# Optimization experiments

Measured on AMD Instinct MI355X. Metric: run time of the kernel, lower is better.

## Reference

```python
import jax, jax.numpy as jnp
import numpy as np

N, E, G = 32768, 262144, 1024
FIN, ED = 32, 8
H, C = 4, 64            # gat_heads, graph_hidden_dim
HC = H * C              # 256
FP_IN, DESC_IN = 2048, 200
GOUT, FPOUT, DOUT = 64, 256, 64
TIN = GOUT + FPOUT + DOUT  # 384
NT = 12
BN_EPS = 1e-5


def bn_eval(x, gamma, beta):
    # eval-mode BatchNorm1d with default running stats (mean=0, var=1)
    inv = 1.0 / jnp.sqrt(1.0 + BN_EPS)
    return x * (gamma * inv) + beta


def gatv2(x, edge_index, edge_attr, Wl, bl, Wr, br, We, att, bias):
    """PyG GATv2Conv (concat heads, add_self_loops=True, fill_value='mean')."""
    n = x.shape[0]
    src, dst = edge_index[0], edge_index[1]
    # self-loop edge_attr = mean of incoming edge_attr per node (PyG fill_value='mean')
    deg = jax.ops.segment_sum(jnp.ones(src.shape, x.dtype), dst, n)
    ea_loop = jax.ops.segment_sum(edge_attr, dst, n) / jnp.maximum(deg, 1.0)[:, None]
    loop = jnp.arange(n)
    src = jnp.concatenate([src, loop])
    dst = jnp.concatenate([dst, loop])
    ea = jnp.concatenate([edge_attr, ea_loop], axis=0)
    xl = (x @ Wl + bl).reshape(n, H, C)   # source transform
    xr = (x @ Wr + br).reshape(n, H, C)   # target transform
    ee = (ea @ We).reshape(-1, H, C)      # edge transform (no bias in PyG)
    m = jax.nn.leaky_relu(xl[src] + xr[dst] + ee, 0.2)  # [E', H, C]
    logit = jnp.einsum('ehc,hc->eh', m, att)            # [E', H]
    # segment softmax over incoming edges of each target node
    lmax = jax.ops.segment_max(logit, dst, n)
    p = jnp.exp(logit - lmax[dst])
    alpha = p / jax.ops.segment_sum(p, dst, n)[dst]
    out = jax.ops.segment_sum(xl[src] * alpha[:, :, None], dst, n)  # [n, H, C]
    return out.reshape(n, HC) + bias


def setup_inputs() -> dict:
    key = jax.random.key(0)
    ks = iter(jax.random.split(key, 64))

    def p(shape, scale=0.05):
        return jax.random.normal(next(ks), shape, dtype=jnp.float32) * scale

    inp = {}
    inp['x'] = jax.random.normal(next(ks), (N, FIN), dtype=jnp.float32)
    inp['edge_index'] = jax.random.randint(next(ks), (2, E), 0, N, dtype=jnp.int32)
    inp['edge_attr'] = jax.random.normal(next(ks), (E, ED), dtype=jnp.float32)
    inp['batch'] = (jnp.arange(N) * G) // N          # sorted, covers all G graphs
    inp['fp'] = jax.random.uniform(next(ks), (G, FP_IN), dtype=jnp.float32)
    inp['desc'] = jax.random.normal(next(ks), (G, DESC_IN), dtype=jnp.float32)
    # GATv2 layer 1 (in=FIN) and layer 2 (in=HC)
    for tag, fin in (('c1', FIN), ('c2', HC)):
        inp[tag + '_Wl'] = p((fin, HC))
        inp[tag + '_bl'] = p((HC,))
        inp[tag + '_Wr'] = p((fin, HC))
        inp[tag + '_br'] = p((HC,))
        inp[tag + '_We'] = p((ED, HC))
        inp[tag + '_att'] = p((H, C))
        inp[tag + '_bias'] = p((HC,))
    inp['gW'], inp['gb'] = p((HC, GOUT)), p((GOUT,))
    inp['g_gn'], inp['g_bt'] = jnp.ones((GOUT,)), jnp.zeros((GOUT,))
    inp['fW'], inp['fb'] = p((FP_IN, FPOUT)), p((FPOUT,))
    inp['f_gn'], inp['f_bt'] = jnp.ones((FPOUT,)), jnp.zeros((FPOUT,))
    inp['dW'], inp['db'] = p((DESC_IN, DOUT)), p((DOUT,))
    inp['d_gn'], inp['d_bt'] = jnp.ones((DOUT,)), jnp.zeros((DOUT,))
    inp['k1W'], inp['k1b'] = p((TIN, TIN // 2)), p((TIN // 2,))
    inp['k1_gn'], inp['k1_bt'] = jnp.ones((TIN // 2,)), jnp.zeros((TIN // 2,))
    inp['k2W'], inp['k2b'] = p((TIN // 2, TIN // 4)), p((TIN // 4,))
    inp['k2_gn'], inp['k2_bt'] = jnp.ones((TIN // 4,)), jnp.zeros((TIN // 4,))
    inp['k3W'], inp['k3b'] = p((TIN // 4, NT)), p((NT,))
    return inp


def reference(x, edge_index, edge_attr, batch, fp, desc,
              c1_Wl, c1_bl, c1_Wr, c1_br, c1_We, c1_att, c1_bias,
              c2_Wl, c2_bl, c2_Wr, c2_br, c2_We, c2_att, c2_bias,
              gW, gb, g_gn, g_bt, fW, fb, f_gn, f_bt, dW, db, d_gn, d_bt,
              k1W, k1b, k1_gn, k1_bt, k2W, k2b, k2_gn, k2_bt, k3W, k3b):
    h = jax.nn.relu(gatv2(x, edge_index, edge_attr, c1_Wl, c1_bl, c1_Wr, c1_br, c1_We, c1_att, c1_bias))
    h = jax.nn.relu(gatv2(h, edge_index, edge_attr, c2_Wl, c2_bl, c2_Wr, c2_br, c2_We, c2_att, c2_bias))
    xg = jax.ops.segment_max(h, batch, G)                 # global_max_pool
    xg = bn_eval(jax.nn.relu(xg @ gW + gb), g_gn, g_bt)
    xf = bn_eval(jax.nn.relu(fp @ fW + fb), f_gn, f_bt)
    xd = bn_eval(jax.nn.relu(desc @ dW + db), d_gn, d_bt)
    z = jnp.concatenate([xg, xf, xd], axis=1)             # [G, TIN]
    z = bn_eval(jax.nn.relu(z @ k1W + k1b), k1_gn, k1_bt)  # dropout off (eval)
    z = bn_eval(jax.nn.relu(z @ k2W + k2b), k2_gn, k2_bt)
    return z @ k3W + k3b                                  # [G, NT]
```

## Files before the change

### kernel.cpp

```cpp
#include <hip/hip_runtime.h>
#include <hip/hip_bf16.h>
#include <math.h>

#define NHEAD 4
#define HC 256

typedef short short8 __attribute__((ext_vector_type(8)));
typedef short short4v __attribute__((ext_vector_type(4)));
typedef float f32x4 __attribute__((ext_vector_type(4)));

__device__ inline f32x4 bf4_to_f32(short4v v)
{
  f32x4 r;
#pragma unroll
  for (int i = 0; i < 4; ++i)
    r[i] = __uint_as_float(((unsigned)(unsigned short)v[i]) << 16);
  return r;
}

__device__ inline float bf_to_f32(unsigned short u)
{
  return __uint_as_float(((unsigned)u) << 16);
}

__device__ inline short4v f4_to_bf4(f32x4 v)
{
  short4v o;
#pragma unroll
  for (int i = 0; i < 4; ++i) {
    __hip_bfloat16 h = __float2bfloat16(v[i]);
    o[i] = *(short*)&h;
  }
  return o;
}

template <int CTRL>
__device__ inline float dpp_radd(float x)
{
  int yi = __builtin_amdgcn_update_dpp(0, __float_as_int(x), CTRL, 0xf, 0xf, true);
  return x + __int_as_float(yi);
}

__global__ void prep_kernel(
    const float* __restrict__ x, const float* __restrict__ fp,
    const float* __restrict__ c1Wl, const float* __restrict__ c1Wr,
    const float* __restrict__ c2Wl, const float* __restrict__ c2Wr,
    const float* __restrict__ desc, const float* __restrict__ dW,
    const float* __restrict__ k1W, const float* __restrict__ fW,
    const int* __restrict__ dst, int* __restrict__ deg,
    __hip_bfloat16* __restrict__ xbf, __hip_bfloat16* __restrict__ fpbf,
    __hip_bfloat16* __restrict__ wt1, __hip_bfloat16* __restrict__ wt2,
    __hip_bfloat16* __restrict__ descbf, __hip_bfloat16* __restrict__ dwt,
    __hip_bfloat16* __restrict__ k1wt, __hip_bfloat16* __restrict__ fwt,
    int N, int G, int E, int DIN)
{
  const int n0 = N * 8;
  const int n1 = G * 512;
  const int n2 = 512 * 32, n3 = 512 * 256;
  const int n4 = G * 224, n5 = 64 * 224, n6 = 192 * 384;
  const int n7 = 256 * 2048;
  int idx = blockIdx.x * 256 + threadIdx.x;
  if (idx < n0) {
    f32x4 v = ((const f32x4*)x)[idx];
    ((short4v*)xbf)[idx] = f4_to_bf4(v);
    return;
  }
  idx -= n0;
  if (idx < n1) {
    f32x4 v = ((const f32x4*)fp)[idx];
    ((short4v*)fpbf)[idx] = f4_to_bf4(v);
    return;
  }
  idx -= n1;
  if (idx < n2) {
    int n = idx / 32, k = idx - n * 32;
    float v = (n < 256) ? c1Wl[k * 256 + n] : c1Wr[k * 256 + (n - 256)];
    wt1[idx] = __float2bfloat16(v); return;
  }
  idx -= n2;
  if (idx < n3) {
    int n = idx / 256, k = idx - n * 256;
    float v = (n < 256) ? c2Wl[k * 256 + n] : c2Wr[k * 256 + (n - 256)];
    wt2[idx] = __float2bfloat16(v); return;
  }
  idx -= n3;
  if (idx < n4) {
    int row = idx / 224, kp = idx - row * 224;
    float v = (kp < DIN) ? desc[(long)row * DIN + kp] : 0.f;
    descbf[idx] = __float2bfloat16(v); return;
  }
  idx -= n4;
  if (idx < n5) {
    int n = idx / 224, kp = idx - n * 224;
    float v = (kp < DIN) ? dW[kp * 64 + n] : 0.f;
    dwt[idx] = __float2bfloat16(v); return;
  }
  idx -= n5;
  if (idx < n6) {
    int n = idx / 384, k = idx - n * 384;
    k1wt[idx] = __float2bfloat16(k1W[k * 192 + n]); return;
  }
  idx -= n6;
  if (idx < n7) {
    int n = idx >> 11, k = idx & 2047;
    fwt[idx] = __float2bfloat16(fW[k * 256 + n]); return;
  }
  idx -= n7;
  if (idx < E) atomicAdd(&deg[dst[idx]], 1);
}

__global__ __launch_bounds__(256) void gemm_mfma_kernel(
    const __hip_bfloat16* __restrict__ A, const __hip_bfloat16* __restrict__ BT,
    const float* __restrict__ bl, const float* __restrict__ br,
    __hip_bfloat16* __restrict__ XL, __hip_bfloat16* __restrict__ XR, int M, int K)
{
  __shared__ short As[128 * 40];
  __shared__ short Bs[128 * 40];
  int bm = blockIdx.x * 128, bn = blockIdx.y * 128;
  int t = threadIdx.x;
  int w = t >> 6, l = t & 63;
  int quad = l >> 4, l16 = l & 15;
  int srow = t >> 1, scol = (t & 1) * 16;

  f32x4 acc[2][8];
#pragma unroll
  for (int i = 0; i < 2; ++i)
#pragma unroll
    for (int j = 0; j < 8; ++j) acc[i][j] = (f32x4){0.f, 0.f, 0.f, 0.f};

  for (int k0 = 0; k0 < K; k0 += 32) {
    *(short8*)&As[srow * 40 + scol] =
        *(const short8*)(const void*)&A[(long)(bm + srow) * K + k0 + scol];
    *(short8*)&As[srow * 40 + scol + 8] =
        *(const short8*)(const void*)&A[(long)(bm + srow) * K + k0 + scol + 8];
    *(short8*)&Bs[srow * 40 + scol] =
        *(const short8*)(const void*)&BT[(long)(bn + srow) * K + k0 + scol];
    *(short8*)&Bs[srow * 40 + scol + 8] =
        *(const short8*)(const void*)&BT[(long)(bn + srow) * K + k0 + scol + 8];
    __syncthreads();
    short8 af[2], bf[8];
#pragma unroll
    for (int mt = 0; mt < 2; ++mt)
      af[mt] = *(short8*)&As[(w * 32 + mt * 16 + l16) * 40 + quad * 8];
#pragma unroll
    for (int nt = 0; nt < 8; ++nt)
      bf[nt] = *(short8*)&Bs[(nt * 16 + l16) * 40 + quad * 8];
#pragma unroll
    for (int mt = 0; mt < 2; ++mt)
#pragma unroll
      for (int nt = 0; nt < 8; ++nt)
        acc[mt][nt] = __builtin_amdgcn_mfma_f32_16x16x32_bf16(af[mt], bf[nt], acc[mt][nt], 0, 0, 0);
    __syncthreads();
  }
#pragma unroll
  for (int mt = 0; mt < 2; ++mt)
#pragma unroll
    for (int nt = 0; nt < 8; ++nt) {
      int col = bn + nt * 16 + l16;
      float b = (col < 256) ? bl[col] : br[col - 256];
#pragma unroll
      for (int r = 0; r < 4; ++r) {
        int row = bm + w * 32 + mt * 16 + quad * 4 + r;
        float v = acc[mt][nt][r] + b;
        if (col < 256)
          XL[(long)row * 256 + col] = __float2bfloat16(v);
        else
          XR[(long)row * 256 + (col - 256)] = __float2bfloat16(v);
      }
    }
}

__global__ __launch_bounds__(256) void gemm_rb_kernel(
    const __hip_bfloat16* __restrict__ A, const __hip_bfloat16* __restrict__ BT,
    const float* __restrict__ bias, const float* __restrict__ gamma,
    const float* __restrict__ beta, void* __restrict__ out,
    int M, int K, int ldc, int coloff, int obf)
{
  __shared__ short As[64 * 40];
  __shared__ short Bs[64 * 40];
  int bm = blockIdx.x * 64, bn = blockIdx.y * 64;
  int t = threadIdx.x;
  int w = t >> 6, l = t & 63;
  int quad = l >> 4, l16 = l & 15;
  int lrow = t >> 2, col8 = (t & 3) * 8;

  f32x4 acc[4];
#pragma unroll
  for (int nt = 0; nt < 4; ++nt) acc[nt] = (f32x4){0.f, 0.f, 0.f, 0.f};

  for (int k0 = 0; k0 < K; k0 += 32) {
    *(short8*)&As[lrow * 40 + col8] =
        *(const short8*)(const void*)&A[(long)(bm + lrow) * K + k0 + col8];
    *(short8*)&Bs[lrow * 40 + col8] =
        *(const short8*)(const void*)&BT[(long)(bn + lrow) * K + k0 + col8];
    __syncthreads();
    short8 af = *(short8*)&As[(w * 16 + l16) * 40 + quad * 8];
#pragma unroll
    for (int nt = 0; nt < 4; ++nt) {
      short8 bf = *(short8*)&Bs[(nt * 16 + l16) * 40 + quad * 8];
      acc[nt] = __builtin_amdgcn_mfma_f32_16x16x32_bf16(af, bf, acc[nt], 0, 0, 0);
    }
    __syncthreads();
  }
  const float inv = rsqrtf(1.f + 1e-5f);
#pragma unroll
  for (int nt = 0; nt < 4; ++nt) {
    int col = bn + nt * 16 + l16;
    float b = bias[col], gm = gamma[col] * inv, bt = beta[col];
#pragma unroll
    for (int r = 0; r < 4; ++r) {
      int row = bm + w * 16 + quad * 4 + r;
      float v = fmaxf(acc[nt][r] + b, 0.f) * gm + bt;
      if (obf)
        ((__hip_bfloat16*)out)[(long)row * ldc + coloff + col] = __float2bfloat16(v);
      else
        ((float*)out)[(long)row * ldc + coloff + col] = v;
    }
  }
}

__global__ __launch_bounds__(256) void mega1_kernel(
    const __hip_bfloat16* __restrict__ fpbf, const __hip_bfloat16* __restrict__ fwt,
    float* __restrict__ P,
    const int* __restrict__ esrc, const int* __restrict__ edst,
    const float* __restrict__ ea, int* __restrict__ cursor,
    int* __restrict__ csr_src, float* __restrict__ csr_ea,
    const __hip_bfloat16* __restrict__ descbf, const __hip_bfloat16* __restrict__ dwt,
    const float* __restrict__ db, const float* __restrict__ d_gn,
    const float* __restrict__ d_bt, __hip_bfloat16* __restrict__ zbuf,
    int G, int E)
{
  __shared__ short As[64 * 40];
  __shared__ short Bs[64 * 40];
  int b = blockIdx.x;
  const int t = threadIdx.x;
  const int NB_SKB = (G / 64) * 16;
  const int NB_FILL = E / 256;

  if (b < NB_SKB) {
    const int gx = G / 64;
    int bx = b % gx, rem = b / gx;
    int by = rem & 3, s = rem >> 2;
    int bm = bx * 64, bn = by * 64;
    const int K = 2048, Kc = 512;
    int kb = s * Kc, ke = kb + Kc;
    int w = t >> 6, l = t & 63;
    int quad = l >> 4, l16 = l & 15;
    int lrow = t >> 2, col8 = (t & 3) * 8;

    f32x4 acc[4];
#pragma unroll
    for (int nt = 0; nt < 4; ++nt) acc[nt] = (f32x4){0.f, 0.f, 0.f, 0.f};

    for (int k0 = kb; k0 < ke; k0 += 32) {
      *(short8*)&As[lrow * 40 + col8] =
          *(const short8*)(const void*)&fpbf[(long)(bm + lrow) * K + k0 + col8];
      *(short8*)&Bs[lrow * 40 + col8] =
          *(const short8*)(const void*)&fwt[(long)(bn + lrow) * K + k0 + col8];
      __syncthreads();
      short8 af = *(short8*)&As[(w * 16 + l16) * 40 + quad * 8];
#pragma unroll
      for (int nt = 0; nt < 4; ++nt) {
        short8 bf = *(short8*)&Bs[(nt * 16 + l16) * 40 + quad * 8];
        acc[nt] = __builtin_amdgcn_mfma_f32_16x16x32_bf16(af, bf, acc[nt], 0, 0, 0);
      }
      __syncthreads();
    }
#pragma unroll
    for (int nt = 0; nt < 4; ++nt) {
      int col = bn + nt * 16 + l16;
#pragma unroll
      for (int r = 0; r < 4; ++r) {
        int row = bm + w * 16 + quad * 4 + r;
        P[((long)s * G + row) * 256 + col] = acc[nt][r];
      }
    }
    return;
  }
  b -= NB_SKB;
  if (b < NB_FILL) {
    int e = b * 256 + t;
    if (e < E) {
      int pos = atomicAdd(&cursor[edst[e]], 1);
      csr_src[pos] = esrc[e];
      f32x4 a0 = *(const f32x4*)(const void*)&ea[(long)e * 8];
      f32x4 a1 = *(const f32x4*)(const void*)&ea[(long)e * 8 + 4];
      *(f32x4*)&csr_ea[(long)pos * 8] = a0;
      *(f32x4*)&csr_ea[(long)pos * 8 + 4] = a1;
    }
    return;
  }
  b -= NB_FILL;
  {
    int bm = b * 64;
    const int K = 224;
    int w = t >> 6, l = t & 63;
    int quad = l >> 4, l16 = l & 15;
    int lrow = t >> 2, col8 = (t & 3) * 8;

    f32x4 acc[4];
#pragma unroll
    for (int nt = 0; nt < 4; ++nt) acc[nt] = (f32x4){0.f, 0.f, 0.f, 0.f};

    for (int k0 = 0; k0 < K; k0 += 32) {
      *(short8*)&As[lrow * 40 + col8] =
          *(const short8*)(const void*)&descbf[(long)(bm + lrow) * K + k0 + col8];
      *(short8*)&Bs[lrow * 40 + col8] =
          *(const short8*)(const void*)&dwt[(long)lrow * K + k0 + col8];
      __syncthreads();
      short8 af = *(short8*)&As[(w * 16 + l16) * 40 + quad * 8];
#pragma unroll
      for (int nt = 0; nt < 4; ++nt) {
        short8 bf = *(short8*)&Bs[(nt * 16 + l16) * 40 + quad * 8];
        acc[nt] = __builtin_amdgcn_mfma_f32_16x16x32_bf16(af, bf, acc[nt], 0, 0, 0);
      }
      __syncthreads();
    }
    const float inv = rsqrtf(1.f + 1e-5f);
#pragma unroll
    for (int nt = 0; nt < 4; ++nt) {
      int col = nt * 16 + l16;
      float bb = db[col], gm = d_gn[col] * inv, bt = d_bt[col];
#pragma unroll
      for (int r = 0; r < 4; ++r) {
        int row = bm + w * 16 + quad * 4 + r;
        float v = fmaxf(acc[nt][r] + bb, 0.f) * gm + bt;
        zbuf[(long)row * 384 + 320 + col] = __float2bfloat16(v);
      }
    }
  }
}

__global__ __launch_bounds__(256) void mega2_kernel(
    const float* __restrict__ csr_ea, const int* __restrict__ csr_ptr,
    float* __restrict__ ea_mean,
    const float* __restrict__ P, const float* __restrict__ fb,
    const float* __restrict__ f_gn, const float* __restrict__ f_bt,
    __hip_bfloat16* __restrict__ zbuf, int N, int G)
{
  int b = blockIdx.x;
  int t = threadIdx.x;
  const int NB_EA = N * 8 / 256;
  if (b < NB_EA) {
    int idx = b * 256 + t;
    int node = idx >> 3, d = idx & 7;
    int p0 = csr_ptr[node], p1 = csr_ptr[node + 1];
    float s = 0.f;
    for (int k = p0; k < p1; ++k) s += csr_ea[(long)k * 8 + d];
    int cnt = p1 - p0;
    ea_mean[idx] = s / (float)(cnt > 1 ? cnt : 1);
    return;
  }
  b -= NB_EA;
  int idx = b * 256 + t;
  int row = idx >> 8, col = idx & 255;
  float v = 0.f;
#pragma unroll
  for (int s = 0; s < 4; ++s) v += P[(long)s * G * 256 + idx];
  const float inv = rsqrtf(1.f + 1e-5f);
  v = fmaxf(v + fb[col], 0.f) * (f_gn[col] * inv) + f_bt[col];
  zbuf[(long)row * 384 + 64 + col] = __float2bfloat16(v);
}

__global__ __launch_bounds__(256) void poolg_kernel(
    const __hip_bfloat16* __restrict__ h, const float* __restrict__ gW,
    const float* __restrict__ gb, const float* __restrict__ g_gn,
    const float* __restrict__ g_bt, __hip_bfloat16* __restrict__ zbuf, int npg)
{
  __shared__ float smax[256];
  __shared__ float sred[256];
  int g = blockIdx.x, t = threadIdx.x;
  const __hip_bfloat16* base = h + (long)g * npg * HC + t;
  float m = -INFINITY;
#pragma unroll 4
  for (int i = 0; i < npg; ++i)
    m = fmaxf(m, bf_to_f32(*(const unsigned short*)&base[(long)i * HC]));
  smax[t] = m;
  __syncthreads();
  int j = t >> 2, part = t & 3;
  float sum = 0.f;
#pragma unroll 4
  for (int k = part * 64; k < part * 64 + 64; ++k)
    sum = fmaf(smax[k], gW[k * 64 + j], sum);
  sred[t] = sum;
  __syncthreads();
  if (t < 64) {
    float v = sred[t * 4] + sred[t * 4 + 1] + sred[t * 4 + 2] + sred[t * 4 + 3];
    const float inv = rsqrtf(1.f + 1e-5f);
    v = fmaxf(v + gb[t], 0.f) * (g_gn[t] * inv) + g_bt[t];
    zbuf[(long)g * 384 + t] = __float2bfloat16(v);
  }
}

__global__ __launch_bounds__(256) void head23_kernel(
    const float* __restrict__ z1, const float* __restrict__ k2W,
    const float* __restrict__ k2b, const float* __restrict__ k2_gn,
    const float* __restrict__ k2_bt, const float* __restrict__ k3W,
    const float* __restrict__ k3b, float* __restrict__ out)
{
  __shared__ float sW[96 * 96];
  __shared__ float s1[8 * 192];
  __shared__ float s2[8 * 96];
  __shared__ float sk3[96 * 12];
  int b = blockIdx.x, t = threadIdx.x;

  for (int i = t; i < 8 * 192; i += 256) s1[i] = z1[(long)b * (8 * 192) + i];
  for (int i = t; i < 96 * 12; i += 256) sk3[i] = k3W[i];

  int row[3], col[3];
  float acc[3] = {0.f, 0.f, 0.f};
#pragma unroll
  for (int o = 0; o < 3; ++o) {
    int idx = o * 256 + t;
    row[o] = idx / 96;
    col[o] = idx - row[o] * 96;
  }

  for (int half = 0; half < 2; ++half) {
    __syncthreads();
    for (int i = t; i < 96 * 96; i += 256)
      sW[i] = k2W[(long)half * 96 * 96 + i];
    __syncthreads();
#pragma unroll 4
    for (int k = 0; k < 96; ++k) {
#pragma unroll
      for (int o = 0; o < 3; ++o)
        acc[o] = fmaf(s1[row[o] * 192 + half * 96 + k], sW[k * 96 + col[o]], acc[o]);
    }
  }

  const float inv = rsqrtf(1.f + 1e-5f);
#pragma unroll
  for (int o = 0; o < 3; ++o) {
    float v = fmaxf(acc[o] + k2b[col[o]], 0.f) * (k2_gn[col[o]] * inv) + k2_bt[col[o]];
    s2[o * 256 + t] = v;
  }
  __syncthreads();
  if (t < 96) {
    int r3 = t / 12, c3 = t - r3 * 12;
    float a = 0.f;
#pragma unroll 4
    for (int k = 0; k < 96; ++k) a = fmaf(s2[r3 * 96 + k], sk3[k * 12 + c3], a);
    out[(long)(b * 8 + r3) * 12 + c3] = a + k3b[c3];
  }
}

__global__ __launch_bounds__(1024) void scan1_kernel(
    const int* __restrict__ deg, int* __restrict__ ptr,
    int* __restrict__ bsum, int N)
{
  __shared__ int s[1024];
  int b = blockIdx.x, t = threadIdx.x;
  int i = b * 1024 + t;
  int v = (i < N) ? deg[i] : 0;
  s[t] = v;
  __syncthreads();
  for (int off = 1; off < 1024; off <<= 1) {
    int x = (t >= off) ? s[t - off] : 0;
    __syncthreads();
    s[t] += x;
    __syncthreads();
  }
  if (i < N) ptr[i] = s[t] - v;
  if (t == 1023) bsum[b] = s[1023];
}

__global__ __launch_bounds__(256) void scan2_kernel(
    const int* __restrict__ bsum, int* __restrict__ ptr,
    int* __restrict__ cursor, int N, int nb)
{
  int i = blockIdx.x * 256 + threadIdx.x;
  if (i > N) return;
  if (i == N) {
    int tot = 0;
    for (int j = 0; j < nb; ++j) tot += bsum[j];
    ptr[N] = tot;
    return;
  }
  int b = i >> 10;
  int offv = 0;
  for (int j = 0; j < b; ++j) offv += bsum[j];
  int v = ptr[i] + offv;
  ptr[i] = v;
  cursor[i] = v;
}

__global__ __launch_bounds__(128) void gat_kernel(
    const __hip_bfloat16* __restrict__ xlb, const __hip_bfloat16* __restrict__ xrb,
    const float* __restrict__ csr_ea, const int* __restrict__ csr_src,
    const int* __restrict__ csr_ptr, const float* __restrict__ ea_mean,
    const float* __restrict__ We, const float* __restrict__ att,
    const float* __restrict__ bias, __hip_bfloat16* __restrict__ out, int N)
{
  int lane = threadIdx.x & 63;
  int node = blockIdx.x * 2 + (threadIdx.x >> 6);
  if (node >= N) return;
  int cbase = (lane >> 4) * 64 + (lane & 15) * 4;

  f32x4 attv = *(const f32x4*)(const void*)&att[cbase];
  f32x4 xriv = bf4_to_f32(*(const short4v*)(const void*)&xrb[(long)node * HC + cbase]);
  f32x4 WeR[8];
#pragma unroll
  for (int d = 0; d < 8; ++d)
    WeR[d] = *(const f32x4*)(const void*)&We[d * HC + cbase];

  float rsumA = 0.f, rsumB = 0.f;
  f32x4 accA = (f32x4){0.f, 0.f, 0.f, 0.f};
  f32x4 accB = (f32x4){0.f, 0.f, 0.f, 0.f};

  int p0 = csr_ptr[node], p1 = csr_ptr[node + 1];

  auto edge_compute = [&](f32x4 xls, f32x4 ea0, f32x4 ea1,
                          float& rsum, f32x4& acc) {
    f32x4 mv = xriv + xls;
#pragma unroll
    for (int d = 0; d < 4; ++d) mv += WeR[d] * ea0[d];
#pragma unroll
    for (int d = 0; d < 4; ++d) mv += WeR[d + 4] * ea1[d];
    float t = 0.f;
#pragma unroll
    for (int r = 0; r < 4; ++r) {
      float m = mv[r];
      m = (m > 0.f) ? m : 0.2f * m;
      t = fmaf(m, attv[r], t);
    }
    t = dpp_radd<0x121>(t);
    t = dpp_radd<0x122>(t);
    t = dpp_radd<0x124>(t);
    t = dpp_radd<0x128>(t);
    float p = __expf(t);
    rsum += p;
    acc += p * xls;
  };

  short4v xA = (short4v){0, 0, 0, 0}, xB = xA, xC = xA;
  f32x4 a0A = (f32x4){0.f, 0.f, 0.f, 0.f}, a1A = a0A;
  f32x4 a0B = a0A, a1B = a0A, a0C = a0A, a1C = a0A;
  int s3A = 0, s3B = 0, s3C = 0;

  int s0 = 0, s1 = 0, s2 = 0;
  if (p0 < p1)     s0 = csr_src[p0];
  if (p0 + 1 < p1) s1 = csr_src[p0 + 1];
  if (p0 + 2 < p1) s2 = csr_src[p0 + 2];
  if (p0 + 3 < p1) s3A = csr_src[p0 + 3];
  if (p0 + 4 < p1) s3B = csr_src[p0 + 4];
  if (p0 + 5 < p1) s3C = csr_src[p0 + 5];
  if (p0 < p1) {
    a0A = *(const f32x4*)(const void*)&csr_ea[(long)p0 * 8];
    a1A = *(const f32x4*)(const void*)&csr_ea[(long)p0 * 8 + 4];
    xA = *(const short4v*)(const void*)&xlb[(long)s0 * HC + cbase];
  }
  if (p0 + 1 < p1) {
    a0B = *(const f32x4*)(const void*)&csr_ea[(long)(p0 + 1) * 8];
    a1B = *(const f32x4*)(const void*)&csr_ea[(long)(p0 + 1) * 8 + 4];
    xB = *(const short4v*)(const void*)&xlb[(long)s1 * HC + cbase];
  }
  if (p0 + 2 < p1) {
    a0C = *(const f32x4*)(const void*)&csr_ea[(long)(p0 + 2) * 8];
    a1C = *(const f32x4*)(const void*)&csr_ea[(long)(p0 + 2) * 8 + 4];
    xC = *(const short4v*)(const void*)&xlb[(long)s2 * HC + cbase];
  }

  int k = p0;
  for (; k + 3 <= p1; k += 3) {
    f32x4 e0 = a0A, e1 = a1A;
    short4v xc = xA;
    if (k + 3 < p1) {
      xA = *(const short4v*)(const void*)&xlb[(long)s3A * HC + cbase];
      a0A = *(const f32x4*)(const void*)&csr_ea[(long)(k + 3) * 8];
      a1A = *(const f32x4*)(const void*)&csr_ea[(long)(k + 3) * 8 + 4];
    }
    if (k + 6 < p1) s3A = csr_src[k + 6];
    edge_compute(bf4_to_f32(xc), e0, e1, rsumA, accA);

    e0 = a0B; e1 = a1B; xc = xB;
    if (k + 4 < p1) {
      xB = *(const short4v*)(const void*)&xlb[(long)s3B * HC + cbase];
      a0B = *(const f32x4*)(const void*)&csr_ea[(long)(k + 4) * 8];
      a1B = *(const f32x4*)(const void*)&csr_ea[(long)(k + 4) * 8 + 4];
    }
    if (k + 7 < p1) s3B = csr_src[k + 7];
    edge_compute(bf4_to_f32(xc), e0, e1, rsumB, accB);

    e0 = a0C; e1 = a1C; xc = xC;
    if (k + 5 < p1) {
      xC = *(const short4v*)(const void*)&xlb[(long)s3C * HC + cbase];
      a0C = *(const f32x4*)(const void*)&csr_ea[(long)(k + 5) * 8];
      a1C = *(const f32x4*)(const void*)&csr_ea[(long)(k + 5) * 8 + 4];
    }
    if (k + 8 < p1) s3C = csr_src[k + 8];
    edge_compute(bf4_to_f32(xc), e0, e1, rsumA, accA);
  }
  if (k < p1)     edge_compute(bf4_to_f32(xA), a0A, a1A, rsumA, accA);
  if (k + 1 < p1) edge_compute(bf4_to_f32(xB), a0B, a1B, rsumB, accB);

  f32x4 em0 = *(const f32x4*)(const void*)&ea_mean[(long)node * 8];
  f32x4 em1 = *(const f32x4*)(const void*)&ea_mean[(long)node * 8 + 4];
  f32x4 xls_self = bf4_to_f32(*(const short4v*)(const void*)&xlb[(long)node * HC + cbase]);
  edge_compute(xls_self, em0, em1, rsumB, accB);

  float invs = 1.f / (rsumA + rsumB);
  f32x4 biasv = *(const f32x4*)(const void*)&bias[cbase];
  short4v pk;
#pragma unroll
  for (int r = 0; r < 4; ++r) {
    float v = fmaxf((accA[r] + accB[r]) * invs + biasv[r], 0.f);
    __hip_bfloat16 hv = __float2bfloat16(v);
    pk[r] = *(short*)&hv;
  }
  *(short4v*)&out[(long)node * HC + cbase] = pk;
}

extern "C" void kernel_launch(void* const* d_in, const int* in_sizes, int n_in,
                              void* d_out, int out_size, void* d_ws, size_t ws_size,
                              hipStream_t stream)
{
  const float* x          = (const float*)d_in[0];
  const int*   edge_index = (const int*)d_in[1];
  const float* edge_attr  = (const float*)d_in[2];
  const float* fp         = (const float*)d_in[4];
  const float* desc       = (const float*)d_in[5];
  const float *c1_Wl = (const float*)d_in[6],  *c1_bl = (const float*)d_in[7],
              *c1_Wr = (const float*)d_in[8],  *c1_br = (const float*)d_in[9],
              *c1_We = (const float*)d_in[10], *c1_att = (const float*)d_in[11],
              *c1_bias = (const float*)d_in[12];
  const float *c2_Wl = (const float*)d_in[13], *c2_bl = (const float*)d_in[14],
              *c2_Wr = (const float*)d_in[15], *c2_br = (const float*)d_in[16],
              *c2_We = (const float*)d_in[17], *c2_att = (const float*)d_in[18],
              *c2_bias = (const float*)d_in[19];
  const float *gW = (const float*)d_in[20], *gb = (const float*)d_in[21],
              *g_gn = (const float*)d_in[22], *g_bt = (const float*)d_in[23];
  const float *fW = (const float*)d_in[24], *fb = (const float*)d_in[25],
              *f_gn = (const float*)d_in[26], *f_bt = (const float*)d_in[27];
  const float *dW = (const float*)d_in[28], *db = (const float*)d_in[29],
              *d_gn = (const float*)d_in[30], *d_bt = (const float*)d_in[31];
  const float *k1W = (const float*)d_in[32], *k1b = (const float*)d_in[33],
              *k1_gn = (const float*)d_in[34], *k1_bt = (const float*)d_in[35];
  const float *k2W = (const float*)d_in[36], *k2b = (const float*)d_in[37],
              *k2_gn = (const float*)d_in[38], *k2_bt = (const float*)d_in[39];
  const float *k3W = (const float*)d_in[40], *k3b = (const float*)d_in[41];

  const int N = in_sizes[0] / 32;
  const int E = in_sizes[1] / 2;
  const int G = in_sizes[4] / 2048;
  const int FIN = 32, FPIN = 2048;
  const int DIN = in_sizes[5] / G;

  char* ws = (char*)d_ws;
  size_t off = 0;
  auto alloc = [&](size_t bytes) {
    void* p = ws + off;
    off = (off + bytes + 255) & ~(size_t)255;
    return p;
  };
  __hip_bfloat16* xlb    = (__hip_bfloat16*)alloc((size_t)N * HC * 2);
  __hip_bfloat16* xrb    = (__hip_bfloat16*)alloc((size_t)N * HC * 2);
  __hip_bfloat16* hb1    = (__hip_bfloat16*)alloc((size_t)N * HC * 2);
  __hip_bfloat16* hb2    = (__hip_bfloat16*)alloc((size_t)N * HC * 2);
  __hip_bfloat16* xbf    = (__hip_bfloat16*)alloc((size_t)N * FIN * 2);
  __hip_bfloat16* fpbf   = (__hip_bfloat16*)alloc((size_t)G * FPIN * 2);
  __hip_bfloat16* wt1    = (__hip_bfloat16*)alloc((size_t)512 * FIN * 2);
  __hip_bfloat16* wt2    = (__hip_bfloat16*)alloc((size_t)512 * HC * 2);
  __hip_bfloat16* fwt    = (__hip_bfloat16*)alloc((size_t)256 * FPIN * 2);
  __hip_bfloat16* descbf = (__hip_bfloat16*)alloc((size_t)G * 224 * 2);
  __hip_bfloat16* dwt    = (__hip_bfloat16*)alloc((size_t)64 * 224 * 2);
  __hip_bfloat16* k1wt   = (__hip_bfloat16*)alloc((size_t)192 * 384 * 2);
  __hip_bfloat16* zbuf   = (__hip_bfloat16*)alloc((size_t)G * 384 * 2);
  float* z1      = (float*)alloc((size_t)G * 192 * 4);
  float* P_fp    = (float*)alloc((size_t)4 * G * 256 * 4);
  int*   deg     = (int*)alloc((size_t)N * 4);
  int*   csr_ptr = (int*)alloc((size_t)(N + 1) * 4);
  int*   cursor  = (int*)alloc((size_t)N * 4);
  int*   csr_src = (int*)alloc((size_t)E * 4);
  float* csr_ea  = (float*)alloc((size_t)E * 8 * 4);
  float* ea_mean = (float*)alloc((size_t)N * 8 * 4);
  int*   bsum    = (int*)alloc((size_t)64 * 4);
  (void)ws_size;

  const int* srcp = edge_index;
  const int* dstp = edge_index + E;
  const int nb = (N + 1023) / 1024;

  hipMemsetAsync(deg, 0, (size_t)N * 4, stream);

  {
    long total = (long)N * 8 + (long)G * 512 + 512 * 32 + 512 * 256 +
                 (long)G * 224 + 64 * 224 + 192 * 384 + 256 * 2048 + E;
    prep_kernel<<<(int)((total + 255) / 256), 256, 0, stream>>>(
        x, fp, c1_Wl, c1_Wr, c2_Wl, c2_Wr, desc, dW, k1W, fW, dstp, deg,
        xbf, fpbf, wt1, wt2, descbf, dwt, k1wt, fwt, N, G, E, DIN);
  }
  scan1_kernel<<<nb, 1024, 0, stream>>>(deg, csr_ptr, bsum, N);
  scan2_kernel<<<(N + 1 + 255) / 256, 256, 0, stream>>>(bsum, csr_ptr, cursor, N, nb);

  {
    int nblk = (G / 64) * 16 + E / 256 + G / 64;
    mega1_kernel<<<nblk, 256, 0, stream>>>(
        fpbf, fwt, P_fp, srcp, dstp, edge_attr, cursor, csr_src, csr_ea,
        descbf, dwt, db, d_gn, d_bt, zbuf, G, E);
  }

  gemm_mfma_kernel<<<dim3(N / 128, 4), 256, 0, stream>>>(xbf, wt1, c1_bl, c1_br, xlb, xrb, N, FIN);

  mega2_kernel<<<N * 8 / 256 + G, 256, 0, stream>>>(
      csr_ea, csr_ptr, ea_mean, P_fp, fb, f_gn, f_bt, zbuf, N, G);

  gat_kernel<<<N / 2, 128, 0, stream>>>(xlb, xrb, csr_ea, csr_src, csr_ptr, ea_mean,
                                        c1_We, c1_att, c1_bias, hb1, N);
  gemm_mfma_kernel<<<dim3(N / 128, 4), 256, 0, stream>>>(hb1, wt2, c2_bl, c2_br, xlb, xrb, N, HC);
  gat_kernel<<<N / 2, 128, 0, stream>>>(xlb, xrb, csr_ea, csr_src, csr_ptr, ea_mean,
                                        c2_We, c2_att, c2_bias, hb2, N);

  poolg_kernel<<<G, 256, 0, stream>>>(hb2, gW, gb, g_gn, g_bt, zbuf, N / G);

  gemm_rb_kernel<<<dim3(G / 64, 3), 256, 0, stream>>>(zbuf, k1wt, k1b, k1_gn, k1_bt,
                                                      z1, G, 384, 192, 0, 0);
  head23_kernel<<<G / 8, 256, 0, stream>>>(z1, k2W, k2b, k2_gn, k2_bt, k3W, k3b,
                                           (float*)d_out);
}
```

Baseline: 388.6 us.

## Fuse layer-1 GEMM into mega1 and collapse pooling plus MLP head into one kernel

Result: slower. 403.0 us (+3.7%).

```diff
diff --git a/kernel.cpp b/kernel.cpp
--- a/kernel.cpp
+++ b/kernel.cpp
@@ -46,19 +46,19 @@
     const float* __restrict__ c1Wl, const float* __restrict__ c1Wr,
     const float* __restrict__ c2Wl, const float* __restrict__ c2Wr,
     const float* __restrict__ desc, const float* __restrict__ dW,
-    const float* __restrict__ k1W, const float* __restrict__ fW,
+    const float* __restrict__ fW,
     const int* __restrict__ dst, int* __restrict__ deg,
     __hip_bfloat16* __restrict__ xbf, __hip_bfloat16* __restrict__ fpbf,
     __hip_bfloat16* __restrict__ wt1, __hip_bfloat16* __restrict__ wt2,
     __hip_bfloat16* __restrict__ descbf, __hip_bfloat16* __restrict__ dwt,
-    __hip_bfloat16* __restrict__ k1wt, __hip_bfloat16* __restrict__ fwt,
+    __hip_bfloat16* __restrict__ fwt,
     int N, int G, int E, int DIN)
 {
   const int n0 = N * 8;
   const int n1 = G * 512;
   const int n2 = 512 * 32, n3 = 512 * 256;
-  const int n4 = G * 224, n5 = 64 * 224, n6 = 192 * 384;
-  const int n7 = 256 * 2048;
+  const int n4 = G * 224, n5 = 64 * 224;
+  const int n6 = 256 * 2048;
   int idx = blockIdx.x * 256 + threadIdx.x;
   if (idx < n0) {
     f32x4 v = ((const f32x4*)x)[idx];
@@ -97,15 +97,10 @@
   }
   idx -= n5;
   if (idx < n6) {
-    int n = idx / 384, k = idx - n * 384;
-    k1wt[idx] = __float2bfloat16(k1W[k * 192 + n]); return;
-  }
-  idx -= n6;
-  if (idx < n7) {
     int n = idx >> 11, k = idx & 2047;
     fwt[idx] = __float2bfloat16(fW[k * 256 + n]); return;
   }
-  idx -= n7;
+  idx -= n6;
   if (idx < E) atomicAdd(&deg[dst[idx]], 1);
 }
 
@@ -170,73 +165,99 @@
     }
 }
 
-__global__ __launch_bounds__(256) void gemm_rb_kernel(
-    const __hip_bfloat16* __restrict__ A, const __hip_bfloat16* __restrict__ BT,
-    const float* __restrict__ bias, const float* __restrict__ gamma,
-    const float* __restrict__ beta, void* __restrict__ out,
-    int M, int K, int ldc, int coloff, int obf)
-{
-  __shared__ short As[64 * 40];
-  __shared__ short Bs[64 * 40];
-  int bm = blockIdx.x * 64, bn = blockIdx.y * 64;
-  int t = threadIdx.x;
-  int w = t >> 6, l = t & 63;
-  int quad = l >> 4, l16 = l & 15;
-  int lrow = t >> 2, col8 = (t & 3) * 8;
-
-  f32x4 acc[4];
-#pragma unroll
-  for (int nt = 0; nt < 4; ++nt) acc[nt] = (f32x4){0.f, 0.f, 0.f, 0.f};
-
-  for (int k0 = 0; k0 < K; k0 += 32) {
-    *(short8*)&As[lrow * 40 + col8] =
-        *(const short8*)(const void*)&A[(long)(bm + lrow) * K + k0 + col8];
-    *(short8*)&Bs[lrow * 40 + col8] =
-        *(const short8*)(const void*)&BT[(long)(bn + lrow) * K + k0 + col8];
-    __syncthreads();
-    short8 af = *(short8*)&As[(w * 16 + l16) * 40 + quad * 8];
-#pragma unroll
-    for (int nt = 0; nt < 4; ++nt) {
-      short8 bf = *(short8*)&Bs[(nt * 16 + l16) * 40 + quad * 8];
-      acc[nt] = __builtin_amdgcn_mfma_f32_16x16x32_bf16(af, bf, acc[nt], 0, 0, 0);
-    }
-    __syncthreads();
-  }
-  const float inv = rsqrtf(1.f + 1e-5f);
-#pragma unroll
-  for (int nt = 0; nt < 4; ++nt) {
-    int col = bn + nt * 16 + l16;
-    float b = bias[col], gm = gamma[col] * inv, bt = beta[col];
-#pragma unroll
-    for (int r = 0; r < 4; ++r) {
-      int row = bm + w * 16 + quad * 4 + r;
-      float v = fmaxf(acc[nt][r] + b, 0.f) * gm + bt;
-      if (obf)
-        ((__hip_bfloat16*)out)[(long)row * ldc + coloff + col] = __float2bfloat16(v);
-      else
-        ((float*)out)[(long)row * ldc + coloff + col] = v;
-    }
-  }
-}
-
 __global__ __launch_bounds__(256) void mega1_kernel(
-    const __hip_bfloat16* __restrict__ fpbf, const __hip_bfloat16* __restrict__ fwt,
-    float* __restrict__ P,
     const int* __restrict__ esrc, const int* __restrict__ edst,
     const float* __restrict__ ea, int* __restrict__ cursor,
     int* __restrict__ csr_src, float* __restrict__ csr_ea,
+    const __hip_bfloat16* __restrict__ xbf, const __hip_bfloat16* __restrict__ wt1,
+    const float* __restrict__ c1_bl, const float* __restrict__ c1_br,
+    __hip_bfloat16* __restrict__ xlb, __hip_bfloat16* __restrict__ xrb,
+    const __hip_bfloat16* __restrict__ fpbf, const __hip_bfloat16* __restrict__ fwt,
+    float* __restrict__ P,
     const __hip_bfloat16* __restrict__ descbf, const __hip_bfloat16* __restrict__ dwt,
     const float* __restrict__ db, const float* __restrict__ d_gn,
     const float* __restrict__ d_bt, __hip_bfloat16* __restrict__ zbuf,
-    int G, int E)
-{
-  __shared__ short As[64 * 40];
-  __shared__ short Bs[64 * 40];
+    int N, int G, int E)
+{
+  __shared__ short As[128 * 40];
+  __shared__ short Bs[128 * 40];
   int b = blockIdx.x;
   const int t = threadIdx.x;
+  const int NB_FILL = E / 256;
+  const int GX1 = N / 128;
+  const int NB_GEMM1 = GX1 * 4;
   const int NB_SKB = (G / 64) * 16;
-  const int NB_FILL = E / 256;
-
+
+  if (b < NB_FILL) {
+    int e = b * 256 + t;
+    if (e < E) {
+      int pos = atomicAdd(&cursor[edst[e]], 1);
+      csr_src[pos] = esrc[e];
+      f32x4 a0 = *(const f32x4*)(const void*)&ea[(long)e * 8];
+      f32x4 a1 = *(const f32x4*)(const void*)&ea[(long)e * 8 + 4];
+      *(f32x4*)&csr_ea[(long)pos * 8] = a0;
+      *(f32x4*)&csr_ea[(long)pos * 8 + 4] = a1;
+    }
+    return;
+  }
+  b -= NB_FILL;
+  if (b < NB_GEMM1) {
+    int bx = b % GX1, by = b / GX1;
+    int bm = bx * 128, bn = by * 128;
+    const int K = 32;
+    int w = t >> 6, l = t & 63;
+    int quad = l >> 4, l16 = l & 15;
+    int srow = t >> 1, scol = (t & 1) * 16;
+
+    f32x4 acc[2][8];
+#pragma unroll
+    for (int i = 0; i < 2; ++i)
+#pragma unroll
+      for (int j = 0; j < 8; ++j) acc[i][j] = (f32x4){0.f, 0.f, 0.f, 0.f};
+
+    {
+      const int k0 = 0;
+      *(short8*)&As[srow * 40 + scol] =
+          *(const short8*)(const void*)&xbf[(long)(bm + srow) * K + k0 + scol];
+      *(short8*)&As[srow * 40 + scol + 8] =
+          *(const short8*)(const void*)&xbf[(long)(bm + srow) * K + k0 + scol + 8];
+      *(short8*)&Bs[srow * 40 + scol] =
+          *(const short8*)(const void*)&wt1[(long)(bn + srow) * K + k0 + scol];
+      *(short8*)&Bs[srow * 40 + scol + 8] =
+          *(const short8*)(const void*)&wt1[(long)(bn + srow) * K + k0 + scol + 8];
+      __syncthreads();
+      short8 af[2], bf[8];
+#pragma unroll
+      for (int mt = 0; mt < 2; ++mt)
+        af[mt] = *(short8*)&As[(w * 32 + mt * 16 + l16) * 40 + quad * 8];
+#pragma unroll
+      for (int nt = 0; nt < 8; ++nt)
+        bf[nt] = *(short8*)&Bs[(nt * 16 + l16) * 40 + quad * 8];
+#pragma unroll
+      for (int mt = 0; mt < 2; ++mt)
+#pragma unroll
+        for (int nt = 0; nt < 8; ++nt)
+          acc[mt][nt] = __builtin_amdgcn_mfma_f32_16x16x32_bf16(af[mt], bf[nt], acc[mt][nt], 0, 0, 0);
+    }
+#pragma unroll
+    for (int mt = 0; mt < 2; ++mt)
+#pragma unroll
+      for (int nt = 0; nt < 8; ++nt) {
+        int col = bn + nt * 16 + l16;
+        float bb = (col < 256) ? c1_bl[col] : c1_br[col - 256];
+#pragma unroll
+        for (int r = 0; r < 4; ++r) {
+          int row = bm + w * 32 + mt * 16 + quad * 4 + r;
+          float v = acc[mt][nt][r] + bb;
+          if (col < 256)
+            xlb[(long)row * 256 + col] = __float2bfloat16(v);
+          else
+            xrb[(long)row * 256 + (col - 256)] = __float2bfloat16(v);
+        }
+      }
+    return;
+  }
+  b -= NB_GEMM1;
   if (b < NB_SKB) {
     const int gx = G / 64;
     int bx = b % gx, rem = b / gx;
@@ -278,19 +299,6 @@
     return;
   }
   b -= NB_SKB;
-  if (b < NB_FILL) {
-    int e = b * 256 + t;
-    if (e < E) {
-      int pos = atomicAdd(&cursor[edst[e]], 1);
-      csr_src[pos] = esrc[e];
-      f32x4 a0 = *(const f32x4*)(const void*)&ea[(long)e * 8];
-      f32x4 a1 = *(const f32x4*)(const void*)&ea[(long)e * 8 + 4];
-      *(f32x4*)&csr_ea[(long)pos * 8] = a0;
-      *(f32x4*)&csr_ea[(long)pos * 8 + 4] = a1;
-    }
-    return;
-  }
-  b -= NB_FILL;
   {
     int bm = b * 64;
     const int K = 224;
@@ -362,21 +370,34 @@
   zbuf[(long)row * 384 + 64 + col] = __float2bfloat16(v);
 }
 
-__global__ __launch_bounds__(256) void poolg_kernel(
+__global__ __launch_bounds__(256) void tailg_kernel(
     const __hip_bfloat16* __restrict__ h, const float* __restrict__ gW,
     const float* __restrict__ gb, const float* __restrict__ g_gn,
-    const float* __restrict__ g_bt, __hip_bfloat16* __restrict__ zbuf, int npg)
+    const float* __restrict__ g_bt, const __hip_bfloat16* __restrict__ zbuf,
+    const float* __restrict__ k1W, const float* __restrict__ k1b,
+    const float* __restrict__ k1_gn, const float* __restrict__ k1_bt,
+    const float* __restrict__ k2W, const float* __restrict__ k2b,
+    const float* __restrict__ k2_gn, const float* __restrict__ k2_bt,
+    const float* __restrict__ k3W, const float* __restrict__ k3b,
+    float* __restrict__ out, int npg)
 {
   __shared__ float smax[256];
   __shared__ float sred[256];
+  __shared__ float sz[384];
+  __shared__ float s1[192];
+  __shared__ float s2[96];
   int g = blockIdx.x, t = threadIdx.x;
+
   const __hip_bfloat16* base = h + (long)g * npg * HC + t;
   float m = -INFINITY;
 #pragma unroll 4
   for (int i = 0; i < npg; ++i)
     m = fmaxf(m, bf_to_f32(*(const unsigned short*)&base[(long)i * HC]));
   smax[t] = m;
+  for (int i = t; i < 320; i += 256)
+    sz[64 + i] = bf_to_f32(*(const unsigned short*)&zbuf[(long)g * 384 + 64 + i]);
   __syncthreads();
+
   int j = t >> 2, part = t & 3;
   float sum = 0.f;
 #pragma unroll 4
@@ -384,64 +405,35 @@
     sum = fmaf(smax[k], gW[k * 64 + j], sum);
   sred[t] = sum;
   __syncthreads();
+  const float inv = rsqrtf(1.f + 1e-5f);
   if (t < 64) {
     float v = sred[t * 4] + sred[t * 4 + 1] + sred[t * 4 + 2] + sred[t * 4 + 3];
-    const float inv = rsqrtf(1.f + 1e-5f);
     v = fmaxf(v + gb[t], 0.f) * (g_gn[t] * inv) + g_bt[t];
-    zbuf[(long)g * 384 + t] = __float2bfloat16(v);
-  }
-}
-
-__global__ __launch_bounds__(256) void head23_kernel(
-    const float* __restrict__ z1, const float* __restrict__ k2W,
-    const float* __restrict__ k2b, const float* __restrict__ k2_gn,
-    const float* __restrict__ k2_bt, const float* __restrict__ k3W,
-    const float* __restrict__ k3b, float* __restrict__ out)
-{
-  __shared__ float sW[96 * 96];
-  __shared__ float s1[8 * 192];
-  __shared__ float s2[8 * 96];
-  __shared__ float sk3[96 * 12];
-  int b = blockIdx.x, t = threadIdx.x;
-
-  for (int i = t; i < 8 * 192; i += 256) s1[i] = z1[(long)b * (8 * 192) + i];
-  for (int i = t; i < 96 * 12; i += 256) sk3[i] = k3W[i];
-
-  int row[3], col[3];
-  float acc[3] = {0.f, 0.f, 0.f};
-#pragma unroll
-  for (int o = 0; o < 3; ++o) {
-    int idx = o * 256 + t;
-    row[o] = idx / 96;
-    col[o] = idx - row[o] * 96;
-  }
-
-  for (int half = 0; half < 2; ++half) {
-    __syncthreads();
-    for (int i = t; i < 96 * 96; i += 256)
-      sW[i] = k2W[(long)half * 96 * 96 + i];
-    __syncthreads();
-#pragma unroll 4
-    for (int k = 0; k < 96; ++k) {
-#pragma unroll
-      for (int o = 0; o < 3; ++o)
-        acc[o] = fmaf(s1[row[o] * 192 + half * 96 + k], sW[k * 96 + col[o]], acc[o]);
-    }
-  }
-
-  const float inv = rsqrtf(1.f + 1e-5f);
-#pragma unroll
-  for (int o = 0; o < 3; ++o) {
-    float v = fmaxf(acc[o] + k2b[col[o]], 0.f) * (k2_gn[col[o]] * inv) + k2_bt[col[o]];
-    s2[o * 256 + t] = v;
+    sz[t] = v;
   }
   __syncthreads();
-  if (t < 96) {
-    int r3 = t / 12, c3 = t - r3 * 12;
+
+  if (t < 192) {
     float a = 0.f;
 #pragma unroll 4
-    for (int k = 0; k < 96; ++k) a = fmaf(s2[r3 * 96 + k], sk3[k * 12 + c3], a);
-    out[(long)(b * 8 + r3) * 12 + c3] = a + k3b[c3];
+    for (int k = 0; k < 384; ++k) a = fmaf(sz[k], k1W[k * 192 + t], a);
+    s1[t] = fmaxf(a + k1b[t], 0.f) * (k1_gn[t] * inv) + k1_bt[t];
+  }
+  __syncthreads();
+
+  if (t < 96) {
+    float a = 0.f;
+#pragma unroll 4
+    for (int k = 0; k < 192; ++k) a = fmaf(s1[k], k2W[k * 96 + t], a);
+    s2[t] = fmaxf(a + k2b[t], 0.f) * (k2_gn[t] * inv) + k2_bt[t];
+  }
+  __syncthreads();
+
+  if (t < 12) {
+    float a = 0.f;
+#pragma unroll 4
+    for (int k = 0; k < 96; ++k) a = fmaf(s2[k], k3W[k * 12 + t], a);
+    out[(long)g * 12 + t] = a + k3b[t];
   }
 }
 
@@ -664,9 +656,7 @@
   __hip_bfloat16* fwt    = (__hip_bfloat16*)alloc((size_t)256 * FPIN * 2);
   __hip_bfloat16* descbf = (__hip_bfloat16*)alloc((size_t)G * 224 * 2);
   __hip_bfloat16* dwt    = (__hip_bfloat16*)alloc((size_t)64 * 224 * 2);
-  __hip_bfloat16* k1wt   = (__hip_bfloat16*)alloc((size_t)192 * 384 * 2);
   __hip_bfloat16* zbuf   = (__hip_bfloat16*)alloc((size_t)G * 384 * 2);
-  float* z1      = (float*)alloc((size_t)G * 192 * 4);
   float* P_fp    = (float*)alloc((size_t)4 * G * 256 * 4);
   int*   deg     = (int*)alloc((size_t)N * 4);
   int*   csr_ptr = (int*)alloc((size_t)(N + 1) * 4);
@@ -685,22 +675,21 @@
 
   {
     long total = (long)N * 8 + (long)G * 512 + 512 * 32 + 512 * 256 +
-                 (long)G * 224 + 64 * 224 + 192 * 384 + 256 * 2048 + E;
+                 (long)G * 224 + 64 * 224 + 256 * 2048 + E;
     prep_kernel<<<(int)((total + 255) / 256), 256, 0, stream>>>(
-        x, fp, c1_Wl, c1_Wr, c2_Wl, c2_Wr, desc, dW, k1W, fW, dstp, deg,
-        xbf, fpbf, wt1, wt2, descbf, dwt, k1wt, fwt, N, G, E, DIN);
+        x, fp, c1_Wl, c1_Wr, c2_Wl, c2_Wr, desc, dW, fW, dstp, deg,
+        xbf, fpbf, wt1, wt2, descbf, dwt, fwt, N, G, E, DIN);
   }
   scan1_kernel<<<nb, 1024, 0, stream>>>(deg, csr_ptr, bsum, N);
   scan2_kernel<<<(N + 1 + 255) / 256, 256, 0, stream>>>(bsum, csr_ptr, cursor, N, nb);
 
   {
-    int nblk = (G / 64) * 16 + E / 256 + G / 64;
+    int nblk = E / 256 + (N / 128) * 4 + (G / 64) * 16 + G / 64;
     mega1_kernel<<<nblk, 256, 0, stream>>>(
-        fpbf, fwt, P_fp, srcp, dstp, edge_attr, cursor, csr_src, csr_ea,
-        descbf, dwt, db, d_gn, d_bt, zbuf, G, E);
-  }
-
-  gemm_mfma_kernel<<<dim3(N / 128, 4), 256, 0, stream>>>(xbf, wt1, c1_bl, c1_br, xlb, xrb, N, FIN);
+        srcp, dstp, edge_attr, cursor, csr_src, csr_ea,
+        xbf, wt1, c1_bl, c1_br, xlb, xrb,
+        fpbf, fwt, P_fp, descbf, dwt, db, d_gn, d_bt, zbuf, N, G, E);
+  }
 
   mega2_kernel<<<N * 8 / 256 + G, 256, 0, stream>>>(
       csr_ea, csr_ptr, ea_mean, P_fp, fb, f_gn, f_bt, zbuf, N, G);
@@ -711,10 +700,8 @@
   gat_kernel<<<N / 2, 128, 0, stream>>>(xlb, xrb, csr_ea, csr_src, csr_ptr, ea_mean,
                                         c2_We, c2_att, c2_bias, hb2, N);
 
-  poolg_kernel<<<G, 256, 0, stream>>>(hb2, gW, gb, g_gn, g_bt, zbuf, N / G);
-
-  gemm_rb_kernel<<<dim3(G / 64, 3), 256, 0, stream>>>(zbuf, k1wt, k1b, k1_gn, k1_bt,
-                                                      z1, G, 384, 192, 0, 0);
-  head23_kernel<<<G / 8, 256, 0, stream>>>(z1, k2W, k2b, k2_gn, k2_bt, k3W, k3b,
-                                           (float*)d_out);
-}
+  tailg_kernel<<<G, 256, 0, stream>>>(hb2, gW, gb, g_gn, g_bt, zbuf,
+                                      k1W, k1b, k1_gn, k1_bt,
+                                      k2W, k2b, k2_gn, k2_bt,
+                                      k3W, k3b, (float*)d_out, N / G);
+}
```
